# Kernel tuning notes

Hardware: AMD Instinct MI355X
Metric: run time of the kernel (lower is better)

## Reference

```python
import jax, jax.numpy as jnp
import numpy as np

N = 50000      # nodes
E = 800000     # edges
D = 128        # input_dim
HID = 128      # hidden_dim
OUT = 128      # output_dim
NH = 16        # n_heads (head_dim = 8)
EF = 16        # edge_feat_dim
RF = 64        # r_feat_dim
KV = 2 * D + EF + RF  # 336


def _ln(x, g, b):
    m = x.mean(-1, keepdims=True)
    v = ((x - m) ** 2).mean(-1, keepdims=True)
    return (x - m) / jnp.sqrt(v + 1e-5) * g + b


def _mlp(x, W1, b1, g, be, W2, b2):
    # Linear -> LayerNorm -> ReLU -> Linear (targetdiff-style MLP, norm=True)
    h = jax.nn.relu(_ln(x @ W1 + b1, g, be))
    return h @ W2 + b2


def setup_inputs() -> dict:
    key = jax.random.key(0)
    ks = jax.random.split(key, 32)

    def w(k, shape, fan_in):
        return (jax.random.normal(k, shape, jnp.float32) / np.sqrt(fan_in)).astype(jnp.float32)

    inp = {
        'h': jax.random.normal(ks[0], (N, D), jnp.float32),
        'rel_x': jax.random.normal(ks[1], (E, 3), jnp.float32),
        'r_feat': jax.random.normal(ks[2], (E, RF), jnp.float32),
        'edge_feat': jax.random.normal(ks[3], (E, EF), jnp.float32),
        'edge_index': jax.random.randint(ks[4], (2, E), 0, N, jnp.int64 if jax.config.jax_enable_x64 else jnp.int32),
        # xk MLP: KV -> HID -> OUT
        'xk_W1': w(ks[5], (KV, HID), KV), 'xk_b1': jnp.zeros((HID,), jnp.float32),
        'xk_g': jnp.ones((HID,), jnp.float32), 'xk_be': jnp.zeros((HID,), jnp.float32),
        'xk_W2': w(ks[6], (HID, OUT), HID), 'xk_b2': jnp.zeros((OUT,), jnp.float32),
        # xv MLP: KV -> HID -> NH
        'xv_W1': w(ks[7], (KV, HID), KV), 'xv_b1': jnp.zeros((HID,), jnp.float32),
        'xv_g': jnp.ones((HID,), jnp.float32), 'xv_be': jnp.zeros((HID,), jnp.float32),
        'xv_W2': w(ks[8], (HID, NH), HID), 'xv_b2': jnp.zeros((NH,), jnp.float32),
        # xq MLP: D -> HID -> OUT
        'xq_W1': w(ks[9], (D, HID), D), 'xq_b1': jnp.zeros((HID,), jnp.float32),
        'xq_g': jnp.ones((HID,), jnp.float32), 'xq_be': jnp.zeros((HID,), jnp.float32),
        'xq_W2': w(ks[10], (HID, OUT), HID), 'xq_b2': jnp.zeros((OUT,), jnp.float32),
        # edge-weight net: Linear(RF,1) + sigmoid
        'ew_W': w(ks[11], (RF, 1), RF), 'ew_b': jnp.zeros((1,), jnp.float32),
    }
    return inp


def reference(h, rel_x, r_feat, edge_feat, edge_index,
              xk_W1, xk_b1, xk_g, xk_be, xk_W2, xk_b2,
              xv_W1, xv_b1, xv_g, xv_be, xv_W2, xv_b2,
              xq_W1, xq_b1, xq_g, xq_be, xq_W2, xq_b2,
              ew_W, ew_b):
    src, dst = edge_index[0], edge_index[1]
    # gather -> MLPs
    kv_input = jnp.concatenate([edge_feat, r_feat, h[dst], h[src]], axis=-1)  # [E, KV]
    k = _mlp(kv_input, xk_W1, xk_b1, xk_g, xk_be, xk_W2, xk_b2).reshape(-1, NH, OUT // NH)
    v = _mlp(kv_input, xv_W1, xv_b1, xv_g, xv_be, xv_W2, xv_b2)              # [E, NH]
    e_w = jax.nn.sigmoid(r_feat @ ew_W + ew_b)                               # [E, 1]
    v = v * e_w
    v = v[:, :, None] * rel_x[:, None, :]                                    # [E, NH, 3]
    q = _mlp(h, xq_W1, xq_b1, xq_g, xq_be, xq_W2, xq_b2).reshape(-1, NH, OUT // NH)
    # scatter-softmax over dst segments
    s = (q[dst] * k).sum(-1) / np.sqrt(OUT // NH)                            # [E, NH]
    smax = jax.ops.segment_max(s, dst, num_segments=N)
    ex = jnp.exp(s - smax[dst])
    den = jax.ops.segment_sum(ex, dst, num_segments=N)
    alpha = ex / den[dst]                                                     # [E, NH]
    m = alpha[:, :, None] * v                                                 # [E, NH, 3]
    out = jax.ops.segment_sum(m, dst, num_segments=N)                         # [N, NH, 3]
    return out.mean(1)                                                        # [N, 3]
```

## Files before the change

kernel.cpp:

```cpp
#include <hip/hip_runtime.h>
#include <hip/hip_bf16.h>

#define NN 50000
#define NE 800000
#define DD 128
#define NHD 16
#define EFD 16
#define RFD 64
#define KVD 336
#define KST 360
#define ME 32
#define HST 136
#define KSS 132

typedef __attribute__((ext_vector_type(8))) short bf16x8;
typedef __attribute__((ext_vector_type(4))) float f32x4;

__device__ __forceinline__ unsigned short f2bf(float f) {
    __hip_bfloat16 h = __float2bfloat16(f);
    return __builtin_bit_cast(unsigned short, h);
}
__device__ __forceinline__ float bf2f(unsigned short u) {
    return __uint_as_float(((unsigned)u) << 16);
}

__global__ __launch_bounds__(256) void prep_wt(
    const float* __restrict__ xkW1, const float* __restrict__ xvW1,
    unsigned short* __restrict__ Wt)
{
    const int n = blockIdx.x;
    const float* W = (n < 128) ? xkW1 : xvW1;
    const int col = n & 127;
    for (int k = threadIdx.x; k < KST; k += 256) {
        float v = (k < KVD) ? W[(size_t)k * 128 + col] : 0.0f;
        Wt[(size_t)n * KST + k] = f2bf(v);
    }
}

__global__ __launch_bounds__(128) void prep_wt2(
    const float* __restrict__ xkW2, const float* __restrict__ xvW2,
    unsigned short* __restrict__ Wt2)
{
    const int n = blockIdx.x;
    const int k = threadIdx.x;
    float v = (n < 128) ? xkW2[(size_t)k * 128 + n]
                        : xvW2[(size_t)k * 16 + (n - 128)];
    Wt2[(size_t)n * 128 + k] = f2bf(v);
}

__global__ __launch_bounds__(256) void prep_hbf(
    const float* __restrict__ h, unsigned short* __restrict__ hb)
{
    const size_t i = ((size_t)blockIdx.x * 256 + threadIdx.x) * 4;
    const float4 f = *(const float4*)&h[i];
    ushort4 o;
    o.x = f2bf(f.x); o.y = f2bf(f.y); o.z = f2bf(f.z); o.w = f2bf(f.w);
    *(ushort4*)&hb[i] = o;
}

__global__ __launch_bounds__(256) void hist_kernel(
    const int* __restrict__ dst, int* __restrict__ deg)
{
    const int i = blockIdx.x * 256 + threadIdx.x;
    if (i < NE) atomicAdd(&deg[dst[i]], 1);
}

__global__ __launch_bounds__(256) void scan_kernel(
    const int* __restrict__ deg, int* __restrict__ off, int* __restrict__ cur)
{
    __shared__ int wsum[4];
    const int t = threadIdx.x;
    const int lane = t & 63;
    const int w = t >> 6;
    int run = 0;
    for (int base = 0; base < NN; base += 256) {
        int v = (base + t < NN) ? deg[base + t] : 0;
        int x = v;
        #pragma unroll
        for (int o2 = 1; o2 < 64; o2 <<= 1) {
            int y = __shfl_up(x, o2);
            if (lane >= o2) x += y;
        }
        if (lane == 63) wsum[w] = x;
        __syncthreads();
        int pre = 0;
        #pragma unroll
        for (int ww = 0; ww < 4; ww++) if (ww < w) pre += wsum[ww];
        const int tot = wsum[0] + wsum[1] + wsum[2] + wsum[3];
        const int excl = run + pre + x - v;
        if (base + t < NN) { off[base + t] = excl; cur[base + t] = excl; }
        run += tot;
        __syncthreads();
    }
    if (t == 0) off[NN] = run;
}

__global__ __launch_bounds__(256) void scatter_kernel(
    const int* __restrict__ dst, const float* __restrict__ rel_x,
    int* __restrict__ cur, int* __restrict__ pos, float* __restrict__ relp)
{
    const int i = blockIdx.x * 256 + threadIdx.x;
    if (i < NE) {
        const int p = atomicAdd(&cur[dst[i]], 1);
        pos[i] = p;
        relp[(size_t)p * 3 + 0] = rel_x[(size_t)i * 3 + 0];
        relp[(size_t)p * 3 + 1] = rel_x[(size_t)i * 3 + 1];
        relp[(size_t)p * 3 + 2] = rel_x[(size_t)i * 3 + 2];
    }
}

__global__ __launch_bounds__(256) void qmlp_kernel(
    const float* __restrict__ h,
    const float* __restrict__ W1, const float* __restrict__ b1,
    const float* __restrict__ g,  const float* __restrict__ be,
    const float* __restrict__ W2, const float* __restrict__ b2,
    unsigned short* __restrict__ q_bf)
{
    __shared__ float hs[16][DD];
    __shared__ float hid[16][DD];
    __shared__ float red[2][8][2][2];
    const int tid  = threadIdx.x;
    const int col  = tid & 127;
    const int half = tid >> 7;
    const int wp   = (tid >> 6) & 1;
    const int n0   = blockIdx.x * 16;

    {
        const float4* src = (const float4*)&h[(size_t)n0 * DD];
        float4* dstp = (float4*)&hs[0][0];
        dstp[tid]       = src[tid];
        dstp[tid + 256] = src[tid + 256];
    }
    __syncthreads();

    float a[8];
    #pragma unroll
    for (int j = 0; j < 8; j++) a[j] = b1[col];
    #pragma unroll 8
    for (int i = 0; i < DD; i++) {
        float w = W1[i * DD + col];
        #pragma unroll
        for (int j = 0; j < 8; j++) a[j] = fmaf(hs[half * 8 + j][i], w, a[j]);
    }

    #pragma unroll
    for (int j = 0; j < 8; j++) {
        float s1 = a[j], s2 = a[j] * a[j];
        #pragma unroll
        for (int off = 32; off > 0; off >>= 1) {
            s1 += __shfl_xor(s1, off);
            s2 += __shfl_xor(s2, off);
        }
        if ((tid & 63) == 0) { red[half][j][0][wp] = s1; red[half][j][1][wp] = s2; }
    }
    __syncthreads();

    const float gg = g[col], bb = be[col];
    #pragma unroll
    for (int j = 0; j < 8; j++) {
        float s1   = red[half][j][0][0] + red[half][j][0][1];
        float s2   = red[half][j][1][0] + red[half][j][1][1];
        float mean = s1 * (1.0f / DD);
        float var  = s2 * (1.0f / DD) - mean * mean;
        float r    = (a[j] - mean) * rsqrtf(var + 1e-5f) * gg + bb;
        hid[half * 8 + j][col] = fmaxf(r, 0.0f);
    }
    __syncthreads();

    float o[8];
    #pragma unroll
    for (int j = 0; j < 8; j++) o[j] = b2[col];
    #pragma unroll 8
    for (int i = 0; i < DD; i++) {
        float w = W2[i * DD + col];
        #pragma unroll
        for (int j = 0; j < 8; j++) o[j] = fmaf(hid[half * 8 + j][i], w, o[j]);
    }
    #pragma unroll
    for (int j = 0; j < 8; j++)
        q_bf[(size_t)(n0 + half * 8 + j) * DD + col] = f2bf(o[j]);
}

union SharedU {
    unsigned short kv[ME * KST];
    struct {
        unsigned short hidk[ME * HST];
        unsigned short hidv[ME * HST];
    } s2;
    float ks[ME * KSS];
};

template<int MODE>
__global__ __launch_bounds__(256, 6) void edge_kernel(
    const unsigned short* __restrict__ h_bf,
    const float* __restrict__ rel_x,
    const float* __restrict__ r_feat,
    const float* __restrict__ edge_feat,
    const int*   __restrict__ e_src,
    const int*   __restrict__ e_dst,
    const int*   __restrict__ pos,
    const unsigned short* __restrict__ Wt,
    const unsigned short* __restrict__ Wt2,
    const float* __restrict__ xk_b1, const float* __restrict__ xk_g,
    const float* __restrict__ xk_be, const float* __restrict__ xk_b2,
    const float* __restrict__ xv_b1, const float* __restrict__ xv_g,
    const float* __restrict__ xv_be, const float* __restrict__ xv_W2,
    const float* __restrict__ xv_b2,
    const float* __restrict__ ew_W,  const float* __restrict__ ew_b,
    const unsigned short* __restrict__ q_bf,
    float* __restrict__ exv,
    float* __restrict__ vwe,
    float* __restrict__ accN)
{
    __shared__ SharedU u;
    __shared__ float v_s[ME][NHD + 1];
    __shared__ float ew_s[ME];
    __shared__ float rel_s[ME][3];
    __shared__ int   dst_s[ME];
    __shared__ int   src_s[ME];
    __shared__ int   pos_s[ME];

    const int tid = threadIdx.x;
    const int e0  = blockIdx.x * ME;

    if (tid < ME) {
        dst_s[tid] = e_dst[e0 + tid];
        src_s[tid] = e_src[e0 + tid];
        if (MODE == 1) pos_s[tid] = pos[e0 + tid];
    } else if (MODE == 0 && tid < ME + ME * 3) {
        int t = tid - ME;
        rel_s[t / 3][t % 3] = rel_x[(size_t)e0 * 3 + t];
    }
    __syncthreads();

    {
        const int e = tid >> 3, p = tid & 7;
        const size_t ge = (size_t)(e0 + e);
        if (p < 4) {
            float part = 0.0f;
            #pragma unroll
            for (int i = 0; i < 4; i++) {
                float4 f = *(const float4*)&r_feat[ge * RFD + p * 16 + i * 4];
                float4 w = *(const float4*)&ew_W[p * 16 + i * 4];
                part += f.x * w.x + f.y * w.y + f.z * w.z + f.w * w.w;
                ushort4 o; o.x = f2bf(f.x); o.y = f2bf(f.y); o.z = f2bf(f.z); o.w = f2bf(f.w);
                *(ushort4*)&u.kv[e * KST + 16 + p * 16 + i * 4] = o;
            }
            part += __shfl_xor(part, 1);
            part += __shfl_xor(part, 2);
            if (p == 0) ew_s[e] = 1.0f / (1.0f + __expf(-(part + ew_b[0])));
        } else {
            float4 f = *(const float4*)&edge_feat[ge * EFD + (p - 4) * 4];
            ushort4 o; o.x = f2bf(f.x); o.y = f2bf(f.y); o.z = f2bf(f.z); o.w = f2bf(f.w);
            *(ushort4*)&u.kv[e * KST + (p - 4) * 4] = o;
        }
        {
            const uint4* hp = (const uint4*)&h_bf[(size_t)dst_s[e] * DD + p * 16];
            uint4* op = (uint4*)&u.kv[e * KST + 80 + p * 16];
            op[0] = hp[0]; op[1] = hp[1];
        }
        {
            const uint4* hp = (const uint4*)&h_bf[(size_t)src_s[e] * DD + p * 16];
            uint4* op = (uint4*)&u.kv[e * KST + 208 + p * 16];
            op[0] = hp[0]; op[1] = hp[1];
        }
        if (p < 2) {
            uint4 z = make_uint4(0, 0, 0, 0);
            *(uint4*)&u.kv[e * KST + 336 + p * 8] = z;
        }
    }
    __syncthreads();

    const int lane  = tid & 63;
    const int wv    = tid >> 6;
    const int half  = wv >> 1;
    const int mhalf = wv & 1;
    const int c15   = lane & 15;
    const int q     = lane >> 4;

    f32x4 acc[8];
    #pragma unroll
    for (int nt = 0; nt < 8; nt++) acc[nt] = (f32x4){0.f, 0.f, 0.f, 0.f};

    {
        const unsigned short* WtH = Wt + (size_t)(half * 128 + c15) * KST;
        const unsigned short* kvA = &u.kv[(mhalf * 16 + c15) * KST];
        for (int ks = 0; ks < 11; ks++) {
            const int k0 = ks * 32 + q * 8;
            bf16x8 a0 = *(const bf16x8*)&kvA[k0];
            #pragma unroll
            for (int nt = 0; nt < 8; nt++) {
                bf16x8 b = *(const bf16x8*)&WtH[(size_t)nt * 16 * KST + k0];
                acc[nt] = __builtin_amdgcn_mfma_f32_16x16x32_bf16(a0, b, acc[nt], 0, 0, 0);
            }
        }
    }

    {
        const float* b1p = half ? xv_b1 : xk_b1;
        const float* gp  = half ? xv_g  : xk_g;
        const float* bep = half ? xv_be : xk_be;
        float bia[8], gam[8], bet[8];
        #pragma unroll
        for (int nt = 0; nt < 8; nt++) {
            int idx = nt * 16 + c15;
            bia[nt] = b1p[idx]; gam[nt] = gp[idx]; bet[nt] = bep[idx];
        }
        #pragma unroll
        for (int r = 0; r < 4; r++) {
            float x[8]; float s1 = 0.f, s2 = 0.f;
            #pragma unroll
            for (int nt = 0; nt < 8; nt++) {
                x[nt] = acc[nt][r] + bia[nt];
                s1 += x[nt]; s2 = fmaf(x[nt], x[nt], s2);
            }
            #pragma unroll
            for (int off = 1; off < 16; off <<= 1) {
                s1 += __shfl_xor(s1, off);
                s2 += __shfl_xor(s2, off);
            }
            float mean = s1 * (1.0f / 128.0f);
            float var  = s2 * (1.0f / 128.0f) - mean * mean;
            float rstd = rsqrtf(var + 1e-5f);
            #pragma unroll
            for (int nt = 0; nt < 8; nt++)
                acc[nt][r] = fmaxf((x[nt] - mean) * rstd * gam[nt] + bet[nt], 0.0f);
        }
    }
    __syncthreads();

    {
        unsigned short* hdst = half ? u.s2.hidv : u.s2.hidk;
        #pragma unroll
        for (int r = 0; r < 4; r++) {
            const int row = mhalf * 16 + q * 4 + r;
            #pragma unroll
            for (int nt = 0; nt < 8; nt++)
                hdst[row * HST + nt * 16 + c15] = f2bf(acc[nt][r]);
        }
    }
    __syncthreads();

    const int mb2 = mhalf * 16;
    const int nb2 = half * 64;
    f32x4 acck[4];
    #pragma unroll
    for (int nt = 0; nt < 4; nt++) acck[nt] = (f32x4){0.f, 0.f, 0.f, 0.f};
    {
        const unsigned short* A0 = &u.s2.hidk[(mb2 + c15) * HST];
        const unsigned short* B0 = &Wt2[(size_t)(nb2 + c15) * 128];
        #pragma unroll
        for (int ks = 0; ks < 4; ks++) {
            const int k0 = ks * 32 + q * 8;
            bf16x8 a0 = *(const bf16x8*)&A0[k0];
            #pragma unroll
            for (int nt = 0; nt < 4; nt++) {
                bf16x8 b = *(const bf16x8*)&B0[(size_t)nt * 16 * 128 + k0];
                acck[nt] = __builtin_amdgcn_mfma_f32_16x16x32_bf16(a0, b, acck[nt], 0, 0, 0);
            }
        }
    }

    float vacc[2];
    #pragma unroll
    for (int p = 0; p < 2; p++) {
        int item = tid + p * 256;
        int e    = item >> 4;
        int col  = item & 15;
        float a = xv_b2[col];
        #pragma unroll 8
        for (int i4 = 0; i4 < 32; i4++) {
            const ushort4 hv = *(const ushort4*)&u.s2.hidv[e * HST + i4 * 4];
            a = fmaf(bf2f(hv.x), xv_W2[(i4 * 4 + 0) * 16 + col], a);
            a = fmaf(bf2f(hv.y), xv_W2[(i4 * 4 + 1) * 16 + col], a);
            a = fmaf(bf2f(hv.z), xv_W2[(i4 * 4 + 2) * 16 + col], a);
            a = fmaf(bf2f(hv.w), xv_W2[(i4 * 4 + 3) * 16 + col], a);
        }
        vacc[p] = a;
    }
    __syncthreads();

    #pragma unroll
    for (int nt = 0; nt < 4; nt++) {
        const float bias = xk_b2[nb2 + nt * 16 + c15];
        #pragma unroll
        for (int r = 0; r < 4; r++)
            u.ks[(mb2 + q * 4 + r) * KSS + nb2 + nt * 16 + c15] =
                acck[nt][r] + bias;
    }
    #pragma unroll
    for (int p = 0; p < 2; p++) {
        int item = tid + p * 256;
        v_s[item >> 4][item & 15] = vacc[p];
    }
    __syncthreads();

    {
        const float inv_s8 = 0.35355339059327373f;
        const int tc2  = tid & 31;
        const int te2  = tid >> 5;
        const int head = tc2 >> 1;
        const int sub  = tc2 & 1;
        #pragma unroll
        for (int e = 0; e < 4; e++) {
            int el  = te2 * 4 + e;
            int dst = dst_s[el];
            const float4  kk = *(const float4*)&u.ks[el * KSS + tc2 * 4];
            const ushort4 qb = *(const ushort4*)&q_bf[(size_t)dst * DD + tc2 * 4];
            float p = bf2f(qb.x) * kk.x + bf2f(qb.y) * kk.y +
                      bf2f(qb.z) * kk.z + bf2f(qb.w) * kk.w;
            p += __shfl_xor(p, 1);
            float ex = __expf(p * inv_s8);
            if (MODE == 1) {
                const size_t pp = (size_t)pos_s[el] * NHD + head;
                if (sub == 0) exv[pp] = ex;
                else          vwe[pp] = v_s[el][head] * ew_s[el] * ex;
            } else {
                float vw = v_s[el][head] * ew_s[el] * ex;
                float* base = &accN[(((size_t)dst * NHD) + head) * 4];
                if (sub == 0) {
                    atomicAdd(base + 0, vw * rel_s[el][0]);
                    atomicAdd(base + 1, vw * rel_s[el][1]);
                } else {
                    atomicAdd(base + 2, vw * rel_s[el][2]);
                    atomicAdd(base + 3, ex);
                }
            }
        }
    }
}

__global__ __launch_bounds__(256) void gather_kernel(
    const int* __restrict__ off,
    const float* __restrict__ exv, const float* __restrict__ vwe,
    const float* __restrict__ relp, float* __restrict__ out)
{
    const int t = threadIdx.x;
    const int g = t >> 4;
    const int h = t & 15;
    const int n = blockIdx.x * 16 + g;
    if (n >= NN) return;
    const int j0 = off[n], j1 = off[n + 1];
    float den = 0.f, sx = 0.f, sy = 0.f, sz = 0.f;
    for (int j = j0; j < j1; j++) {
        const float ex = exv[(size_t)j * NHD + h];
        const float vw = vwe[(size_t)j * NHD + h];
        const float rx = relp[(size_t)j * 3 + 0];
        const float ry = relp[(size_t)j * 3 + 1];
        const float rz = relp[(size_t)j * 3 + 2];
        sx = fmaf(vw, rx, sx);
        sy = fmaf(vw, ry, sy);
        sz = fmaf(vw, rz, sz);
        den += ex;
    }
    const float c = (den > 0.f) ? 1.0f / den : 0.0f;
    float ox = sx * c, oy = sy * c, oz = sz * c;
    #pragma unroll
    for (int o2 = 1; o2 < 16; o2 <<= 1) {
        ox += __shfl_xor(ox, o2);
        oy += __shfl_xor(oy, o2);
        oz += __shfl_xor(oz, o2);
    }
    if (h == 0) {
        out[(size_t)n * 3 + 0] = ox * (1.0f / NHD);
        out[(size_t)n * 3 + 1] = oy * (1.0f / NHD);
        out[(size_t)n * 3 + 2] = oz * (1.0f / NHD);
    }
}

__global__ __launch_bounds__(256) void finalize_kernel(
    const float* __restrict__ accN, float* __restrict__ out)
{
    int n = blockIdx.x * blockDim.x + threadIdx.x;
    if (n >= NN) return;
    float ox = 0.0f, oy = 0.0f, oz = 0.0f;
    #pragma unroll
    for (int hh = 0; hh < NHD; hh++) {
        float4 a = *(const float4*)&accN[(((size_t)n * NHD) + hh) * 4];
        if (a.w > 0.0f) {
            float r = 1.0f / a.w;
            ox = fmaf(a.x, r, ox);
            oy = fmaf(a.y, r, oy);
            oz = fmaf(a.z, r, oz);
        }
    }
    out[n * 3 + 0] = ox * (1.0f / NHD);
    out[n * 3 + 1] = oy * (1.0f / NHD);
    out[n * 3 + 2] = oz * (1.0f / NHD);
}

extern "C" void kernel_launch(void* const* d_in, const int* in_sizes, int n_in,
                              void* d_out, int out_size, void* d_ws, size_t ws_size,
                              hipStream_t stream)
{
    const float* h         = (const float*)d_in[0];
    const float* rel_x     = (const float*)d_in[1];
    const float* r_feat    = (const float*)d_in[2];
    const float* edge_feat = (const float*)d_in[3];
    const int*   e_idx     = (const int*)d_in[4];
    const float* xk_W1 = (const float*)d_in[5];
    const float* xk_b1 = (const float*)d_in[6];
    const float* xk_g  = (const float*)d_in[7];
    const float* xk_be = (const float*)d_in[8];
    const float* xk_W2 = (const float*)d_in[9];
    const float* xk_b2 = (const float*)d_in[10];
    const float* xv_W1 = (const float*)d_in[11];
    const float* xv_b1 = (const float*)d_in[12];
    const float* xv_g  = (const float*)d_in[13];
    const float* xv_be = (const float*)d_in[14];
    const float* xv_W2 = (const float*)d_in[15];
    const float* xv_b2 = (const float*)d_in[16];
    const float* xq_W1 = (const float*)d_in[17];
    const float* xq_b1 = (const float*)d_in[18];
    const float* xq_g  = (const float*)d_in[19];
    const float* xq_be = (const float*)d_in[20];
    const float* xq_W2 = (const float*)d_in[21];
    const float* xq_b2 = (const float*)d_in[22];
    const float* ew_W  = (const float*)d_in[23];
    const float* ew_b  = (const float*)d_in[24];

    size_t o = 0;
    auto take = [&](size_t bytes) -> char* {
        o = (o + 255) & ~(size_t)255;
        char* p = (char*)d_ws + o;
        o += bytes;
        return p;
    };
    unsigned short* h_bf = (unsigned short*)take((size_t)NN * DD * 2);
    unsigned short* q_bf = (unsigned short*)take((size_t)NN * DD * 2);
    unsigned short* Wt   = (unsigned short*)take((size_t)256 * KST * 2);
    unsigned short* Wt2  = (unsigned short*)take((size_t)144 * 128 * 2);
    int*   deg  = (int*)take((size_t)NN * 4);
    int*   cur  = (int*)take((size_t)NN * 4);
    int*   offv = (int*)take((size_t)(NN + 1) * 4);
    int*   pos  = (int*)take((size_t)NE * 4);
    float* relp = (float*)take((size_t)NE * 3 * 4);
    float* exv  = (float*)take((size_t)NE * NHD * 4);
    float* vwe  = (float*)take((size_t)NE * NHD * 4);
    const bool sorted = (o <= ws_size);
    float* accN = (float*)(void*)deg;

    prep_hbf<<<(NN * DD / 4 + 255) / 256, 256, 0, stream>>>(h, h_bf);
    prep_wt<<<256, 256, 0, stream>>>(xk_W1, xv_W1, Wt);
    prep_wt2<<<144, 128, 0, stream>>>(xk_W2, xv_W2, Wt2);
    qmlp_kernel<<<NN / 16, 256, 0, stream>>>(h, xq_W1, xq_b1, xq_g, xq_be,
                                             xq_W2, xq_b2, q_bf);

    if (sorted) {
        hipMemsetAsync(deg, 0, (size_t)NN * 4, stream);
        hist_kernel<<<(NE + 255) / 256, 256, 0, stream>>>(e_idx + NE, deg);
        scan_kernel<<<1, 256, 0, stream>>>(deg, offv, cur);
        scatter_kernel<<<(NE + 255) / 256, 256, 0, stream>>>(
            e_idx + NE, rel_x, cur, pos, relp);

        edge_kernel<1><<<NE / ME, 256, 0, stream>>>(
            h_bf, rel_x, r_feat, edge_feat,
            e_idx, e_idx + NE, pos,
            Wt, Wt2,
            xk_b1, xk_g, xk_be, xk_b2,
            xv_b1, xv_g, xv_be, xv_W2, xv_b2,
            ew_W, ew_b, q_bf, exv, vwe, nullptr);

        gather_kernel<<<(NN + 15) / 16, 256, 0, stream>>>(
            offv, exv, vwe, relp, (float*)d_out);
    } else {
        hipMemsetAsync(accN, 0, (size_t)NN * NHD * 4 * sizeof(float), stream);
        edge_kernel<0><<<NE / ME, 256, 0, stream>>>(
            h_bf, rel_x, r_feat, edge_feat,
            e_idx, e_idx + NE, nullptr,
            Wt, Wt2,
            xk_b1, xk_g, xk_be, xk_b2,
            xv_b1, xv_g, xv_be, xv_W2, xv_b2,
            ew_W, ew_b, q_bf, nullptr, nullptr, accN);

        finalize_kernel<<<(NN + 255) / 256, 256, 0, stream>>>(accN, (float*)d_out);
    }
}
```

Measured before the change: 1.757 ms.

## Double edges per block and re-lay weights into k-slabs for MFMA reuse

Raises the edge tile from 32 to 64 edges per block, so each wave computes two 16-row M tiles and every weight fragment loaded from global memory feeds two MFMAs. The bf16 weight matrices are rearranged into 32-wide k-slabs so each wave's B-fragment loads are contiguous. The cost is a larger shared tile and more accumulator registers, and the occupancy hint drops from 6 to 3 blocks per CU. Gather, softmax and scatter loops are widened to cover the extra edges.

Measured after the change: 1.417 ms. 19.4% less time.

```diff
diff --git a/kernel.cpp b/kernel.cpp
--- a/kernel.cpp
+++ b/kernel.cpp
@@ -9,9 +9,11 @@
 #define RFD 64
 #define KVD 336
 #define KST 360
-#define ME 32
+#define ME 64
 #define HST 136
 #define KSS 132
+#define WTSLAB 8192
+#define WT2SLAB 4608
 
 typedef __attribute__((ext_vector_type(8))) short bf16x8;
 typedef __attribute__((ext_vector_type(4))) float f32x4;
@@ -31,9 +33,9 @@
     const int n = blockIdx.x;
     const float* W = (n < 128) ? xkW1 : xvW1;
     const int col = n & 127;
-    for (int k = threadIdx.x; k < KST; k += 256) {
+    for (int k = threadIdx.x; k < 352; k += 256) {
         float v = (k < KVD) ? W[(size_t)k * 128 + col] : 0.0f;
-        Wt[(size_t)n * KST + k] = f2bf(v);
+        Wt[(size_t)(k >> 5) * WTSLAB + n * 32 + (k & 31)] = f2bf(v);
     }
 }
 
@@ -45,7 +47,7 @@
     const int k = threadIdx.x;
     float v = (n < 128) ? xkW2[(size_t)k * 128 + n]
                         : xvW2[(size_t)k * 16 + (n - 128)];
-    Wt2[(size_t)n * 128 + k] = f2bf(v);
+    Wt2[(size_t)(k >> 5) * WT2SLAB + n * 32 + (k & 31)] = f2bf(v);
 }
 
 __global__ __launch_bounds__(256) void prep_hbf(
@@ -191,7 +193,7 @@
 };
 
 template<int MODE>
-__global__ __launch_bounds__(256, 6) void edge_kernel(
+__global__ __launch_bounds__(256, 3) void edge_kernel(
     const unsigned short* __restrict__ h_bf,
     const float* __restrict__ rel_x,
     const float* __restrict__ r_feat,
@@ -227,16 +229,21 @@
         dst_s[tid] = e_dst[e0 + tid];
         src_s[tid] = e_src[e0 + tid];
         if (MODE == 1) pos_s[tid] = pos[e0 + tid];
-    } else if (MODE == 0 && tid < ME + ME * 3) {
+    } else if (MODE == 0) {
         int t = tid - ME;
         rel_s[t / 3][t % 3] = rel_x[(size_t)e0 * 3 + t];
     }
     __syncthreads();
 
     {
-        const int e = tid >> 3, p = tid & 7;
+        const int e = tid >> 2, p = tid & 3;
         const size_t ge = (size_t)(e0 + e);
-        if (p < 4) {
+        {
+            float4 f = *(const float4*)&edge_feat[ge * EFD + p * 4];
+            ushort4 o; o.x = f2bf(f.x); o.y = f2bf(f.y); o.z = f2bf(f.z); o.w = f2bf(f.w);
+            *(ushort4*)&u.kv[e * KST + p * 4] = o;
+        }
+        {
             float part = 0.0f;
             #pragma unroll
             for (int i = 0; i < 4; i++) {
@@ -249,20 +256,18 @@
             part += __shfl_xor(part, 1);
             part += __shfl_xor(part, 2);
             if (p == 0) ew_s[e] = 1.0f / (1.0f + __expf(-(part + ew_b[0])));
-        } else {
-            float4 f = *(const float4*)&edge_feat[ge * EFD + (p - 4) * 4];
-            ushort4 o; o.x = f2bf(f.x); o.y = f2bf(f.y); o.z = f2bf(f.z); o.w = f2bf(f.w);
-            *(ushort4*)&u.kv[e * KST + (p - 4) * 4] = o;
         }
         {
-            const uint4* hp = (const uint4*)&h_bf[(size_t)dst_s[e] * DD + p * 16];
-            uint4* op = (uint4*)&u.kv[e * KST + 80 + p * 16];
-            op[0] = hp[0]; op[1] = hp[1];
+            const uint4* hp = (const uint4*)&h_bf[(size_t)dst_s[e] * DD + p * 32];
+            uint4* op = (uint4*)&u.kv[e * KST + 80 + p * 32];
+            #pragma unroll
+            for (int i = 0; i < 4; i++) op[i] = hp[i];
         }
         {
-            const uint4* hp = (const uint4*)&h_bf[(size_t)src_s[e] * DD + p * 16];
-            uint4* op = (uint4*)&u.kv[e * KST + 208 + p * 16];
-            op[0] = hp[0]; op[1] = hp[1];
+            const uint4* hp = (const uint4*)&h_bf[(size_t)src_s[e] * DD + p * 32];
+            uint4* op = (uint4*)&u.kv[e * KST + 208 + p * 32];
+            #pragma unroll
+            for (int i = 0; i < 4; i++) op[i] = hp[i];
         }
         if (p < 2) {
             uint4 z = make_uint4(0, 0, 0, 0);
@@ -271,27 +276,32 @@
     }
     __syncthreads();
 
-    const int lane  = tid & 63;
-    const int wv    = tid >> 6;
-    const int half  = wv >> 1;
-    const int mhalf = wv & 1;
-    const int c15   = lane & 15;
-    const int q     = lane >> 4;
-
-    f32x4 acc[8];
-    #pragma unroll
-    for (int nt = 0; nt < 8; nt++) acc[nt] = (f32x4){0.f, 0.f, 0.f, 0.f};
+    const int lane = tid & 63;
+    const int wv   = tid >> 6;
+    const int half = wv >> 1;
+    const int mrow = (wv & 1) * 32;
+    const int c15  = lane & 15;
+    const int q    = lane >> 4;
+
+    f32x4 acc[2][8];
+    #pragma unroll
+    for (int mt = 0; mt < 2; mt++)
+        #pragma unroll
+        for (int nt = 0; nt < 8; nt++) acc[mt][nt] = (f32x4){0.f, 0.f, 0.f, 0.f};
 
     {
-        const unsigned short* WtH = Wt + (size_t)(half * 128 + c15) * KST;
-        const unsigned short* kvA = &u.kv[(mhalf * 16 + c15) * KST];
+        const unsigned short* WtL = Wt + ((half * 128 + c15) * 32 + q * 8);
+        const unsigned short* kvA = &u.kv[(mrow + c15) * KST];
         for (int ks = 0; ks < 11; ks++) {
             const int k0 = ks * 32 + q * 8;
             bf16x8 a0 = *(const bf16x8*)&kvA[k0];
+            bf16x8 a1 = *(const bf16x8*)&kvA[16 * KST + k0];
+            const unsigned short* Wks = WtL + (size_t)ks * WTSLAB;
             #pragma unroll
             for (int nt = 0; nt < 8; nt++) {
-                bf16x8 b = *(const bf16x8*)&WtH[(size_t)nt * 16 * KST + k0];
-                acc[nt] = __builtin_amdgcn_mfma_f32_16x16x32_bf16(a0, b, acc[nt], 0, 0, 0);
+                bf16x8 b = *(const bf16x8*)&Wks[nt * 512];
+                acc[0][nt] = __builtin_amdgcn_mfma_f32_16x16x32_bf16(a0, b, acc[0][nt], 0, 0, 0);
+                acc[1][nt] = __builtin_amdgcn_mfma_f32_16x16x32_bf16(a1, b, acc[1][nt], 0, 0, 0);
             }
         }
     }
@@ -307,63 +317,73 @@
             bia[nt] = b1p[idx]; gam[nt] = gp[idx]; bet[nt] = bep[idx];
         }
         #pragma unroll
-        for (int r = 0; r < 4; r++) {
-            float x[8]; float s1 = 0.f, s2 = 0.f;
-            #pragma unroll
-            for (int nt = 0; nt < 8; nt++) {
-                x[nt] = acc[nt][r] + bia[nt];
-                s1 += x[nt]; s2 = fmaf(x[nt], x[nt], s2);
+        for (int mt = 0; mt < 2; mt++)
+            #pragma unroll
+            for (int r = 0; r < 4; r++) {
+                float x[8]; float s1 = 0.f, s2 = 0.f;
+                #pragma unroll
+                for (int nt = 0; nt < 8; nt++) {
+                    x[nt] = acc[mt][nt][r] + bia[nt];
+                    s1 += x[nt]; s2 = fmaf(x[nt], x[nt], s2);
+                }
+                #pragma unroll
+                for (int off = 1; off < 16; off <<= 1) {
+                    s1 += __shfl_xor(s1, off);
+                    s2 += __shfl_xor(s2, off);
+                }
+                float mean = s1 * (1.0f / 128.0f);
+                float var  = s2 * (1.0f / 128.0f) - mean * mean;
+                float rstd = rsqrtf(var + 1e-5f);
+                #pragma unroll
+                for (int nt = 0; nt < 8; nt++)
+                    acc[mt][nt][r] = fmaxf((x[nt] - mean) * rstd * gam[nt] + bet[nt], 0.0f);
             }
-            #pragma unroll
-            for (int off = 1; off < 16; off <<= 1) {
-                s1 += __shfl_xor(s1, off);
-                s2 += __shfl_xor(s2, off);
-            }
-            float mean = s1 * (1.0f / 128.0f);
-            float var  = s2 * (1.0f / 128.0f) - mean * mean;
-            float rstd = rsqrtf(var + 1e-5f);
-            #pragma unroll
-            for (int nt = 0; nt < 8; nt++)
-                acc[nt][r] = fmaxf((x[nt] - mean) * rstd * gam[nt] + bet[nt], 0.0f);
-        }
     }
     __syncthreads();
 
     {
         unsigned short* hdst = half ? u.s2.hidv : u.s2.hidk;
         #pragma unroll
-        for (int r = 0; r < 4; r++) {
-            const int row = mhalf * 16 + q * 4 + r;
-            #pragma unroll
-            for (int nt = 0; nt < 8; nt++)
-                hdst[row * HST + nt * 16 + c15] = f2bf(acc[nt][r]);
-        }
-    }
-    __syncthreads();
-
-    const int mb2 = mhalf * 16;
-    const int nb2 = half * 64;
-    f32x4 acck[4];
-    #pragma unroll
-    for (int nt = 0; nt < 4; nt++) acck[nt] = (f32x4){0.f, 0.f, 0.f, 0.f};
+        for (int mt = 0; mt < 2; mt++)
+            #pragma unroll
+            for (int r = 0; r < 4; r++) {
+                const int row = mrow + mt * 16 + q * 4 + r;
+                #pragma unroll
+                for (int nt = 0; nt < 8; nt++)
+                    hdst[row * HST + nt * 16 + c15] = f2bf(acc[mt][nt][r]);
+            }
+    }
+    __syncthreads();
+
+    const int mb2 = (wv & 1) * 32;
+    const int nb2 = (wv >> 1) * 64;
+    f32x4 acck[2][4];
+    #pragma unroll
+    for (int mt = 0; mt < 2; mt++)
+        #pragma unroll
+        for (int nt = 0; nt < 4; nt++) acck[mt][nt] = (f32x4){0.f, 0.f, 0.f, 0.f};
     {
         const unsigned short* A0 = &u.s2.hidk[(mb2 + c15) * HST];
-        const unsigned short* B0 = &Wt2[(size_t)(nb2 + c15) * 128];
+        const unsigned short* A1 = &u.s2.hidk[(mb2 + 16 + c15) * HST];
+        const unsigned short* W2L = Wt2 + ((nb2 + c15) * 32 + q * 8);
         #pragma unroll
         for (int ks = 0; ks < 4; ks++) {
             const int k0 = ks * 32 + q * 8;
             bf16x8 a0 = *(const bf16x8*)&A0[k0];
+            bf16x8 a1 = *(const bf16x8*)&A1[k0];
+            const unsigned short* Wk = W2L + ks * WT2SLAB;
             #pragma unroll
             for (int nt = 0; nt < 4; nt++) {
-                bf16x8 b = *(const bf16x8*)&B0[(size_t)nt * 16 * 128 + k0];
-                acck[nt] = __builtin_amdgcn_mfma_f32_16x16x32_bf16(a0, b, acck[nt], 0, 0, 0);
+                bf16x8 b = *(const bf16x8*)&Wk[nt * 512];
+                acck[0][nt] = __builtin_amdgcn_mfma_f32_16x16x32_bf16(a0, b, acck[0][nt], 0, 0, 0);
+                acck[1][nt] = __builtin_amdgcn_mfma_f32_16x16x32_bf16(a1, b, acck[1][nt], 0, 0, 0);
             }
         }
     }
 
-    float vacc[2];
-    #pragma unroll
-    for (int p = 0; p < 2; p++) {
+    float vacc[4];
+    #pragma unroll
+    for (int p = 0; p < 4; p++) {
         int item = tid + p * 256;
         int e    = item >> 4;
         int col  = item & 15;
@@ -384,12 +404,14 @@
     for (int nt = 0; nt < 4; nt++) {
         const float bias = xk_b2[nb2 + nt * 16 + c15];
         #pragma unroll
-        for (int r = 0; r < 4; r++)
-            u.ks[(mb2 + q * 4 + r) * KSS + nb2 + nt * 16 + c15] =
-                acck[nt][r] + bias;
-    }
-    #pragma unroll
-    for (int p = 0; p < 2; p++) {
+        for (int mt = 0; mt < 2; mt++)
+            #pragma unroll
+            for (int r = 0; r < 4; r++)
+                u.ks[(mb2 + mt * 16 + q * 4 + r) * KSS + nb2 + nt * 16 + c15] =
+                    acck[mt][nt][r] + bias;
+    }
+    #pragma unroll
+    for (int p = 0; p < 4; p++) {
         int item = tid + p * 256;
         v_s[item >> 4][item & 15] = vacc[p];
     }
@@ -402,8 +424,8 @@
         const int head = tc2 >> 1;
         const int sub  = tc2 & 1;
         #pragma unroll
-        for (int e = 0; e < 4; e++) {
-            int el  = te2 * 4 + e;
+        for (int e = 0; e < 8; e++) {
+            int el  = te2 * 8 + e;
             int dst = dst_s[el];
             const float4  kk = *(const float4*)&u.ks[el * KSS + tc2 * 4];
             const ushort4 qb = *(const ushort4*)&q_bf[(size_t)dst * DD + tc2 * 4];
@@ -528,8 +550,8 @@
     };
     unsigned short* h_bf = (unsigned short*)take((size_t)NN * DD * 2);
     unsigned short* q_bf = (unsigned short*)take((size_t)NN * DD * 2);
-    unsigned short* Wt   = (unsigned short*)take((size_t)256 * KST * 2);
-    unsigned short* Wt2  = (unsigned short*)take((size_t)144 * 128 * 2);
+    unsigned short* Wt   = (unsigned short*)take((size_t)11 * WTSLAB * 2);
+    unsigned short* Wt2  = (unsigned short*)take((size_t)4 * WT2SLAB * 2);
     int*   deg  = (int*)take((size_t)NN * 4);
     int*   cur  = (int*)take((size_t)NN * 4);
     int*   offv = (int*)take((size_t)(NN + 1) * 4);
```
